# Performance work log

Measured on AMD Instinct MI355X. Metric: run time of the kernel, lower is better.

## Reference

```python
import jax, jax.numpy as jnp
import numpy as np

N_NODES = 100000
N_EDGES = 1600000
IN_CH = 256
OUT_CH = 128
EPS = 1e-12


def setup_inputs() -> dict:
    key = jax.random.key(0)
    k1, k2, k3 = jax.random.split(key, 3)
    x = jax.random.normal(k1, (N_NODES, IN_CH), dtype=jnp.float32)
    edge_index = jax.random.randint(k2, (2, N_EDGES), 0, N_NODES, dtype=jnp.int64)
    W = jax.random.normal(k3, (IN_CH, OUT_CH), dtype=jnp.float32) / np.float32(np.sqrt(IN_CH))
    b = jnp.zeros((OUT_CH,), dtype=jnp.float32)
    return {"x": x, "edge_index": edge_index, "W": W, "b": b}


def reference(x, edge_index, W, b):
    n = x.shape[0]
    # GCNConv: linear transform first, then normalized aggregation with self-loops
    h = x @ W  # [N, out]
    loops = jnp.arange(n, dtype=edge_index.dtype)
    row = jnp.concatenate([edge_index[0], loops])  # source nodes
    col = jnp.concatenate([edge_index[1], loops])  # destination nodes
    deg = jax.ops.segment_sum(jnp.ones_like(col, dtype=h.dtype), col, num_segments=n)
    dinv = jnp.where(deg > 0, jax.lax.rsqrt(jnp.maximum(deg, 1.0)), 0.0)  # deg^-1/2, inf->0
    wgt = dinv[row] * dinv[col]  # symmetric normalization per edge
    agg = jax.ops.segment_sum(h[row] * wgt[:, None], col, num_segments=n) + b  # [N, out]
    # min-max scale per node (dim=1)
    zmin = agg.min(axis=1, keepdims=True)
    zmax = agg.max(axis=1, keepdims=True)
    z = (agg - zmin) / (zmax - zmin)
    # F.normalize: L2 along dim=1 with eps clamp
    nrm = jnp.maximum(jnp.linalg.norm(z, axis=1, keepdims=True), EPS)
    return z / nrm
```

## Files before the change

kernel.cpp:

```cpp
#include <hip/hip_runtime.h>
#include <hip/hip_bf16.h>

#define N_NODES 100000
#define N_EDGES 1600000
#define IN_CH 256
#define OUT_CH 128

#define BSZ 512
#define NBUCK 196
#define BCAP 9216
#define CSC 8192

#define GEMM_ROWS 32

typedef __attribute__((ext_vector_type(8))) short short8;
typedef __attribute__((ext_vector_type(4))) float floatx4;
typedef __attribute__((ext_vector_type(2))) float float2v;

union bfu { __hip_bfloat16 b; unsigned short u; };

__device__ inline unsigned short f2bf(float v) {
    bfu cv; cv.b = __float2bfloat16(v); return cv.u;
}
__device__ inline float bf2f(unsigned short u) {
    bfu cv; cv.u = u; return __bfloat162float(cv.b);
}

__device__ inline void pkacc(float2v& acc, unsigned g) {
    float2v v;
    v.x = __uint_as_float(g << 16);
    v.y = __uint_as_float(g & 0xffff0000u);
    asm("v_pk_add_f32 %0, %1, %2" : "=v"(acc) : "v"(v), "v"(acc));
}

__global__ __launch_bounds__(256) void pa_scatter(const int* __restrict__ rows,
                                                  const int* __restrict__ cols,
                                                  int* __restrict__ bcursor,
                                                  unsigned* __restrict__ ebuf) {
    __shared__ int lcnt[NBUCK];
    __shared__ int lbase[NBUCK];
    int t = threadIdx.x;
    if (t < NBUCK) lcnt[t] = 0;
    __syncthreads();
    int s0 = blockIdx.x * CSC;
    int e1 = min(N_EDGES, s0 + CSC);
    for (int i = s0 + t; i < e1; i += 256) atomicAdd(&lcnt[cols[i] >> 9], 1);
    __syncthreads();
    if (t < NBUCK) {
        int c = lcnt[t];
        lbase[t] = c ? atomicAdd(&bcursor[t], c) : 0;
        lcnt[t] = 0;
    }
    __syncthreads();
    for (int i = s0 + t; i < e1; i += 256) {
        int c = cols[i], r = rows[i];
        int bk = c >> 9;
        int rank = atomicAdd(&lcnt[bk], 1);
        ebuf[bk * BCAP + lbase[bk] + rank] = ((unsigned)(c & (BSZ - 1)) << 17) | (unsigned)r;
    }
}

__global__ __launch_bounds__(256) void pb_build(const unsigned* __restrict__ ebuf,
                                                const int* __restrict__ bcursor,
                                                int* __restrict__ cnt,
                                                int* __restrict__ base,
                                                float* __restrict__ dinv,
                                                int* __restrict__ es) {
    __shared__ int nh[BSZ];
    __shared__ int sc[BSZ];
    __shared__ int lcur[BSZ];
    int t = threadIdx.x;
    int bk = blockIdx.x;
    int bb = bk * BCAP;
    int bc = bcursor[bk];
    nh[t] = 0; nh[t + 256] = 0;
    lcur[t] = 0; lcur[t + 256] = 0;
    __syncthreads();
    for (int i = t; i < bc; i += 256) atomicAdd(&nh[ebuf[bb + i] >> 17], 1);
    __syncthreads();
    sc[t] = nh[t]; sc[t + 256] = nh[t + 256];
    __syncthreads();
    for (int off = 1; off < BSZ; off <<= 1) {
        int v0 = (t >= off) ? sc[t - off] : 0;
        int i1 = t + 256;
        int v1 = (i1 >= off) ? sc[i1 - off] : 0;
        __syncthreads();
        sc[t] += v0; sc[i1] += v1;
        __syncthreads();
    }
#pragma unroll
    for (int q = 0; q < 2; ++q) {
        int dl = t + q * 256;
        int node = bk * BSZ + dl;
        if (node < N_NODES) {
            int c = nh[dl];
            cnt[node] = c;
            base[node] = bb + sc[dl] - c;
            dinv[node] = rsqrtf((float)(c + 1));
        }
    }
    for (int i = t; i < bc; i += 256) {
        unsigned v = ebuf[bb + i];
        int dl = v >> 17;
        int src = (int)(v & 0x1FFFFu);
        int rank = atomicAdd(&lcur[dl], 1);
        es[bb + sc[dl] - nh[dl] + rank] = src << 8;
    }
}

__global__ void k_prep_w(const float* __restrict__ W,
                         unsigned short* __restrict__ wb_hi,
                         unsigned short* __restrict__ wb_lo) {
    int t = blockIdx.x * 256 + threadIdx.x;
    if (t >= IN_CH * OUT_CH) return;
    int j = t & 7;
    int lane = (t >> 3) & 63;
    int s = (t >> 9) & 7;
    int nt = t >> 12;
    int k = s * 32 + (lane >> 4) * 8 + j;
    int n = nt * 16 + (lane & 15);
    float w = W[k * OUT_CH + n];
    unsigned short hi = f2bf(w);
    wb_hi[t] = hi;
    wb_lo[t] = f2bf(w - bf2f(hi));
}

__global__ __launch_bounds__(512) void k_gemm(const float* __restrict__ x,
                                              const unsigned short* __restrict__ wb_hi,
                                              const unsigned short* __restrict__ wb_lo,
                                              const float* __restrict__ dinv,
                                              unsigned short* __restrict__ hbs) {
    __shared__ short8 xbh[1024];
    __shared__ short8 xbl[1024];
    int t = threadIdx.x;
    int wv = t >> 6;
    int lane = t & 63;
    int row0 = blockIdx.x * GEMM_ROWS;

    short8 Bh[8], Bl[8];
    const short8* bhp = (const short8*)wb_hi + (size_t)wv * 8 * 64 + lane;
    const short8* blp = (const short8*)wb_lo + (size_t)wv * 8 * 64 + lane;
#pragma unroll
    for (int s = 0; s < 8; ++s) {
        Bh[s] = bhp[s * 64];
        Bl[s] = blp[s * 64];
    }

#pragma unroll
    for (int q = 0; q < 2; ++q) {
        int slot = q * 512 + t;
        int ms = slot >> 9;
        int s  = (slot >> 6) & 7;
        int l  = slot & 63;
        int row = row0 + ms * 16 + (l & 15);
        int col = s * 32 + (l >> 4) * 8;
        const float4* xp = (const float4*)(x + (size_t)row * IN_CH + col);
        float4 v0 = xp[0];
        float4 v1 = xp[1];
        float xv[8] = {v0.x, v0.y, v0.z, v0.w, v1.x, v1.y, v1.z, v1.w};
        short8 hh, ll;
#pragma unroll
        for (int j = 0; j < 8; ++j) {
            unsigned short hi = f2bf(xv[j]);
            hh[j] = (short)hi;
            ll[j] = (short)f2bf(xv[j] - bf2f(hi));
        }
        xbh[slot] = hh;
        xbl[slot] = ll;
    }
    __syncthreads();

    int r15 = lane & 15;
    int quad = lane >> 4;

    floatx4 acc[2];
#pragma unroll
    for (int ms = 0; ms < 2; ++ms) {
        acc[ms] = (floatx4){0.f, 0.f, 0.f, 0.f};
#pragma unroll
        for (int s = 0; s < 8; ++s) {
            short8 ah = xbh[(ms * 8 + s) * 64 + lane];
            short8 al = xbl[(ms * 8 + s) * 64 + lane];
            acc[ms] = __builtin_amdgcn_mfma_f32_16x16x32_bf16(ah, Bh[s], acc[ms], 0, 0, 0);
            acc[ms] = __builtin_amdgcn_mfma_f32_16x16x32_bf16(ah, Bl[s], acc[ms], 0, 0, 0);
            acc[ms] = __builtin_amdgcn_mfma_f32_16x16x32_bf16(al, Bh[s], acc[ms], 0, 0, 0);
        }
    }

#pragma unroll
    for (int ms = 0; ms < 2; ++ms)
#pragma unroll
        for (int r = 0; r < 4; ++r) {
            int row = row0 + ms * 16 + quad * 4 + r;
            size_t idx = (size_t)row * OUT_CH + wv * 16 + r15;
            hbs[idx] = f2bf(acc[ms][r] * dinv[row]);
        }
}

__global__ __launch_bounds__(256) void k_agg_fin(const unsigned short* __restrict__ hbs,
                                                 const float* __restrict__ dinv,
                                                 const int* __restrict__ es,
                                                 const int* __restrict__ base,
                                                 const int* __restrict__ cnt,
                                                 const float* __restrict__ b,
                                                 float* __restrict__ out) {
    int t = threadIdx.x;
    int lane = t & 63;
    int ll = lane & 15;
    int node = blockIdx.x * 16 + (t >> 4);

    const char* hb = (const char*)hbs;
    int lane_byte = ll << 4;
    int bidx = (lane & 48) << 2;

    float dn = dinv[node];
    int d  = cnt[node];
    int st = base[node];

    float4 bv0 = ((const float4*)b)[ll * 2];
    float4 bv1 = ((const float4*)b)[ll * 2 + 1];

    uint4 gs = *(const uint4*)(hb + ((size_t)node << 8) + lane_byte);
    float2v acc[4];
    acc[0].x = __uint_as_float(gs.x << 16); acc[0].y = __uint_as_float(gs.x & 0xffff0000u);
    acc[1].x = __uint_as_float(gs.y << 16); acc[1].y = __uint_as_float(gs.y & 0xffff0000u);
    acc[2].x = __uint_as_float(gs.z << 16); acc[2].y = __uint_as_float(gs.z & 0xffff0000u);
    acc[3].x = __uint_as_float(gs.w << 16); acc[3].y = __uint_as_float(gs.w & 0xffff0000u);

    int dm = d;
    dm = max(dm, __shfl_xor(dm, 16, 64));
    dm = max(dm, __shfl_xor(dm, 32, 64));
    int iters = __builtin_amdgcn_readfirstlane((dm + 15) >> 4);

    const int zoff = N_NODES << 8;

    for (int it = 0; it < iters; ++it) {
        int jb = it << 4;
        int off = zoff;
        if (jb + ll < d) off = es[st + jb + ll];

        uint4 ga[4], gb[4];
#pragma unroll
        for (int k = 0; k < 4; ++k) {
            int ro = __builtin_amdgcn_ds_bpermute(bidx + (k << 2), off);
            ga[k] = *(const uint4*)(hb + (unsigned)(ro + lane_byte));
        }
#pragma unroll
        for (int k = 0; k < 4; ++k) {
            int ro = __builtin_amdgcn_ds_bpermute(bidx + ((4 + k) << 2), off);
            gb[k] = *(const uint4*)(hb + (unsigned)(ro + lane_byte));
        }
#pragma unroll
        for (int k = 0; k < 4; ++k) {
            pkacc(acc[0], ga[k].x); pkacc(acc[1], ga[k].y);
            pkacc(acc[2], ga[k].z); pkacc(acc[3], ga[k].w);
        }
#pragma unroll
        for (int k = 0; k < 4; ++k) {
            int ro = __builtin_amdgcn_ds_bpermute(bidx + ((8 + k) << 2), off);
            ga[k] = *(const uint4*)(hb + (unsigned)(ro + lane_byte));
        }
#pragma unroll
        for (int k = 0; k < 4; ++k) {
            pkacc(acc[0], gb[k].x); pkacc(acc[1], gb[k].y);
            pkacc(acc[2], gb[k].z); pkacc(acc[3], gb[k].w);
        }
#pragma unroll
        for (int k = 0; k < 4; ++k) {
            int ro = __builtin_amdgcn_ds_bpermute(bidx + ((12 + k) << 2), off);
            gb[k] = *(const uint4*)(hb + (unsigned)(ro + lane_byte));
        }
#pragma unroll
        for (int k = 0; k < 4; ++k) {
            pkacc(acc[0], ga[k].x); pkacc(acc[1], ga[k].y);
            pkacc(acc[2], ga[k].z); pkacc(acc[3], ga[k].w);
        }
#pragma unroll
        for (int k = 0; k < 4; ++k) {
            pkacc(acc[0], gb[k].x); pkacc(acc[1], gb[k].y);
            pkacc(acc[2], gb[k].z); pkacc(acc[3], gb[k].w);
        }
    }

    float v[8];
    v[0] = dn * acc[0].x + bv0.x;  v[1] = dn * acc[0].y + bv0.y;
    v[2] = dn * acc[1].x + bv0.z;  v[3] = dn * acc[1].y + bv0.w;
    v[4] = dn * acc[2].x + bv1.x;  v[5] = dn * acc[2].y + bv1.y;
    v[6] = dn * acc[3].x + bv1.z;  v[7] = dn * acc[3].y + bv1.w;

    float lmin = v[0], lmax = v[0];
#pragma unroll
    for (int i = 1; i < 8; ++i) { lmin = fminf(lmin, v[i]); lmax = fmaxf(lmax, v[i]); }
#pragma unroll
    for (int m = 8; m; m >>= 1) {
        lmin = fminf(lmin, __shfl_xor(lmin, m, 64));
        lmax = fmaxf(lmax, __shfl_xor(lmax, m, 64));
    }
    float scale = 1.0f / (lmax - lmin);
    float z[8];
    float ss = 0.f;
#pragma unroll
    for (int i = 0; i < 8; ++i) { z[i] = (v[i] - lmin) * scale; ss += z[i] * z[i]; }
#pragma unroll
    for (int m = 8; m; m >>= 1) ss += __shfl_xor(ss, m, 64);
    float inv = 1.0f / fmaxf(sqrtf(ss), 1e-12f);

    float4 o0 = {z[0] * inv, z[1] * inv, z[2] * inv, z[3] * inv};
    float4 o1 = {z[4] * inv, z[5] * inv, z[6] * inv, z[7] * inv};
    float4* op = (float4*)(out + (size_t)node * OUT_CH);
    op[ll * 2] = o0;
    op[ll * 2 + 1] = o1;
}

extern "C" void kernel_launch(void* const* d_in, const int* in_sizes, int n_in,
                              void* d_out, int out_size, void* d_ws, size_t ws_size,
                              hipStream_t stream) {
    const float* x = (const float*)d_in[0];
    const int* ei = (const int*)d_in[1];
    const float* W = (const float*)d_in[2];
    const float* b = (const float*)d_in[3];
    float* out = (float*)d_out;

    char* ws = (char*)d_ws;
    size_t o = 0;
    auto alloc = [&](size_t bytes) { void* p = ws + o; o = (o + bytes + 255) & ~(size_t)255; return p; };
    float* dinv    = (float*)alloc((size_t)N_NODES * 4);
    int*   cnt     = (int*)  alloc((size_t)N_NODES * 4);
    int*   base    = (int*)  alloc((size_t)N_NODES * 4);
    int*   bcursor = (int*)  alloc(NBUCK * 4);
    unsigned short* wb_hi = (unsigned short*)alloc((size_t)IN_CH * OUT_CH * 2);
    unsigned short* wb_lo = (unsigned short*)alloc((size_t)IN_CH * OUT_CH * 2);
    unsigned short* hbs = (unsigned short*)alloc((size_t)(N_NODES + 1) * OUT_CH * 2);
    unsigned* ebuf = (unsigned*)alloc((size_t)NBUCK * BCAP * 4);
    int*   es      = (int*)  alloc((size_t)NBUCK * BCAP * 4);

    const int* rows = ei;
    const int* cols = ei + N_EDGES;

    hipMemsetAsync(bcursor, 0, NBUCK * sizeof(int), stream);
    hipMemsetAsync(hbs + (size_t)N_NODES * OUT_CH, 0, OUT_CH * 2, stream);
    pa_scatter<<<(N_EDGES + CSC - 1) / CSC, 256, 0, stream>>>(rows, cols, bcursor, ebuf);
    pb_build<<<NBUCK, 256, 0, stream>>>(ebuf, bcursor, cnt, base, dinv, es);

    k_prep_w<<<(IN_CH * OUT_CH + 255) / 256, 256, 0, stream>>>(W, wb_hi, wb_lo);
    k_gemm<<<N_NODES / GEMM_ROWS, 512, 0, stream>>>(x, wb_hi, wb_lo, dinv, hbs);

    k_agg_fin<<<N_NODES / 16, 256, 0, stream>>>(hbs, dinv, es, base, cnt, b, out);
}
```

Baseline: 307.4 us.

## Shrink CSR buckets, fold memsets into prep kernel, pad GEMM LDS tile

Halves the bucket size used to build the destination-sorted edge list (391 buckets of 256 nodes) and runs the scatter and build kernels with 512 threads, which gives more parallel blocks in the build stage. The two hipMemsetAsync calls are replaced by zeroing bcursor and the padding row inside k_prep_w, which now runs first and removes extra stream operations. The GEMM now loads x rows with coalesced contiguous reads and stores them into a padded LDS layout (stride 17 per quad) to avoid bank conflicts on the MFMA operand reads. In exchange, smaller buckets mean more global atomics on the bucket cursors, and the GEMM uses slightly more shared memory.

Result: faster. 284.2 us (-7.6%).

```diff
diff --git a/kernel.cpp b/kernel.cpp
--- a/kernel.cpp
+++ b/kernel.cpp
@@ -6,10 +6,10 @@
 #define IN_CH 256
 #define OUT_CH 128
 
-#define BSZ 512
-#define NBUCK 196
-#define BCAP 9216
-#define CSC 8192
+#define BSZ 256
+#define NBUCK 391
+#define BCAP 4736
+#define CSC 4096
 
 #define GEMM_ROWS 32
 
@@ -33,7 +33,33 @@
     asm("v_pk_add_f32 %0, %1, %2" : "=v"(acc) : "v"(v), "v"(acc));
 }
 
-__global__ __launch_bounds__(256) void pa_scatter(const int* __restrict__ rows,
+__global__ void k_prep_w(const float* __restrict__ W,
+                         unsigned short* __restrict__ wb_hi,
+                         unsigned short* __restrict__ wb_lo,
+                         int* __restrict__ bcursor,
+                         unsigned* __restrict__ zrow) {
+    int tid = threadIdx.x;
+    if (blockIdx.x == 0) {
+        if (tid < NBUCK) bcursor[tid] = 0;
+        if (tid + 256 < NBUCK) bcursor[tid + 256] = 0;
+    }
+    if (blockIdx.x == 1 && tid < 64) zrow[tid] = 0;
+
+    int t = blockIdx.x * 256 + tid;
+    if (t >= IN_CH * OUT_CH) return;
+    int j = t & 7;
+    int lane = (t >> 3) & 63;
+    int s = (t >> 9) & 7;
+    int nt = t >> 12;
+    int k = s * 32 + (lane >> 4) * 8 + j;
+    int n = nt * 16 + (lane & 15);
+    float w = W[k * OUT_CH + n];
+    unsigned short hi = f2bf(w);
+    wb_hi[t] = hi;
+    wb_lo[t] = f2bf(w - bf2f(hi));
+}
+
+__global__ __launch_bounds__(512) void pa_scatter(const int* __restrict__ rows,
                                                   const int* __restrict__ cols,
                                                   int* __restrict__ bcursor,
                                                   unsigned* __restrict__ ebuf) {
@@ -44,7 +70,7 @@
     __syncthreads();
     int s0 = blockIdx.x * CSC;
     int e1 = min(N_EDGES, s0 + CSC);
-    for (int i = s0 + t; i < e1; i += 256) atomicAdd(&lcnt[cols[i] >> 9], 1);
+    for (int i = s0 + t; i < e1; i += 512) atomicAdd(&lcnt[cols[i] >> 8], 1);
     __syncthreads();
     if (t < NBUCK) {
         int c = lcnt[t];
@@ -52,15 +78,15 @@
         lcnt[t] = 0;
     }
     __syncthreads();
-    for (int i = s0 + t; i < e1; i += 256) {
+    for (int i = s0 + t; i < e1; i += 512) {
         int c = cols[i], r = rows[i];
-        int bk = c >> 9;
+        int bk = c >> 8;
         int rank = atomicAdd(&lcnt[bk], 1);
         ebuf[bk * BCAP + lbase[bk] + rank] = ((unsigned)(c & (BSZ - 1)) << 17) | (unsigned)r;
     }
 }
 
-__global__ __launch_bounds__(256) void pb_build(const unsigned* __restrict__ ebuf,
+__global__ __launch_bounds__(512) void pb_build(const unsigned* __restrict__ ebuf,
                                                 const int* __restrict__ bcursor,
                                                 int* __restrict__ cnt,
                                                 int* __restrict__ base,
@@ -73,33 +99,28 @@
     int bk = blockIdx.x;
     int bb = bk * BCAP;
     int bc = bcursor[bk];
-    nh[t] = 0; nh[t + 256] = 0;
-    lcur[t] = 0; lcur[t + 256] = 0;
-    __syncthreads();
-    for (int i = t; i < bc; i += 256) atomicAdd(&nh[ebuf[bb + i] >> 17], 1);
-    __syncthreads();
-    sc[t] = nh[t]; sc[t + 256] = nh[t + 256];
+    if (t < BSZ) { nh[t] = 0; lcur[t] = 0; }
+    __syncthreads();
+    for (int i = t; i < bc; i += 512) atomicAdd(&nh[ebuf[bb + i] >> 17], 1);
+    __syncthreads();
+    if (t < BSZ) sc[t] = nh[t];
     __syncthreads();
     for (int off = 1; off < BSZ; off <<= 1) {
-        int v0 = (t >= off) ? sc[t - off] : 0;
-        int i1 = t + 256;
-        int v1 = (i1 >= off) ? sc[i1 - off] : 0;
+        int v = (t < BSZ && t >= off) ? sc[t - off] : 0;
         __syncthreads();
-        sc[t] += v0; sc[i1] += v1;
+        if (t < BSZ) sc[t] += v;
         __syncthreads();
     }
-#pragma unroll
-    for (int q = 0; q < 2; ++q) {
-        int dl = t + q * 256;
-        int node = bk * BSZ + dl;
+    if (t < BSZ) {
+        int node = bk * BSZ + t;
         if (node < N_NODES) {
-            int c = nh[dl];
+            int c = nh[t];
             cnt[node] = c;
-            base[node] = bb + sc[dl] - c;
+            base[node] = bb + sc[t] - c;
             dinv[node] = rsqrtf((float)(c + 1));
         }
     }
-    for (int i = t; i < bc; i += 256) {
+    for (int i = t; i < bc; i += 512) {
         unsigned v = ebuf[bb + i];
         int dl = v >> 17;
         int src = (int)(v & 0x1FFFFu);
@@ -108,30 +129,13 @@
     }
 }
 
-__global__ void k_prep_w(const float* __restrict__ W,
-                         unsigned short* __restrict__ wb_hi,
-                         unsigned short* __restrict__ wb_lo) {
-    int t = blockIdx.x * 256 + threadIdx.x;
-    if (t >= IN_CH * OUT_CH) return;
-    int j = t & 7;
-    int lane = (t >> 3) & 63;
-    int s = (t >> 9) & 7;
-    int nt = t >> 12;
-    int k = s * 32 + (lane >> 4) * 8 + j;
-    int n = nt * 16 + (lane & 15);
-    float w = W[k * OUT_CH + n];
-    unsigned short hi = f2bf(w);
-    wb_hi[t] = hi;
-    wb_lo[t] = f2bf(w - bf2f(hi));
-}
-
 __global__ __launch_bounds__(512) void k_gemm(const float* __restrict__ x,
                                               const unsigned short* __restrict__ wb_hi,
                                               const unsigned short* __restrict__ wb_lo,
                                               const float* __restrict__ dinv,
                                               unsigned short* __restrict__ hbs) {
-    __shared__ short8 xbh[1024];
-    __shared__ short8 xbl[1024];
+    __shared__ short8 xbh[2 * 8 * 68];
+    __shared__ short8 xbl[2 * 8 * 68];
     int t = threadIdx.x;
     int wv = t >> 6;
     int lane = t & 63;
@@ -148,13 +152,10 @@
 
 #pragma unroll
     for (int q = 0; q < 2; ++q) {
-        int slot = q * 512 + t;
-        int ms = slot >> 9;
-        int s  = (slot >> 6) & 7;
-        int l  = slot & 63;
-        int row = row0 + ms * 16 + (l & 15);
-        int col = s * 32 + (l >> 4) * 8;
-        const float4* xp = (const float4*)(x + (size_t)row * IN_CH + col);
+        int c = q * 512 + t;
+        int row = c >> 5;
+        int cc  = c & 31;
+        const float4* xp = (const float4*)(x + (size_t)(row0 + row) * IN_CH + cc * 8);
         float4 v0 = xp[0];
         float4 v1 = xp[1];
         float xv[8] = {v0.x, v0.y, v0.z, v0.w, v1.x, v1.y, v1.z, v1.w};
@@ -165,13 +166,16 @@
             hh[j] = (short)hi;
             ll[j] = (short)f2bf(xv[j] - bf2f(hi));
         }
-        xbh[slot] = hh;
-        xbl[slot] = ll;
+        int ms = row >> 4, r15 = row & 15, s = cc >> 2, q2 = cc & 3;
+        int idx = (ms * 8 + s) * 68 + q2 * 17 + r15;
+        xbh[idx] = hh;
+        xbl[idx] = ll;
     }
     __syncthreads();
 
     int r15 = lane & 15;
     int quad = lane >> 4;
+    int lidx = quad * 17 + r15;
 
     floatx4 acc[2];
 #pragma unroll
@@ -179,8 +183,8 @@
         acc[ms] = (floatx4){0.f, 0.f, 0.f, 0.f};
 #pragma unroll
         for (int s = 0; s < 8; ++s) {
-            short8 ah = xbh[(ms * 8 + s) * 64 + lane];
-            short8 al = xbl[(ms * 8 + s) * 64 + lane];
+            short8 ah = xbh[(ms * 8 + s) * 68 + lidx];
+            short8 al = xbl[(ms * 8 + s) * 68 + lidx];
             acc[ms] = __builtin_amdgcn_mfma_f32_16x16x32_bf16(ah, Bh[s], acc[ms], 0, 0, 0);
             acc[ms] = __builtin_amdgcn_mfma_f32_16x16x32_bf16(ah, Bl[s], acc[ms], 0, 0, 0);
             acc[ms] = __builtin_amdgcn_mfma_f32_16x16x32_bf16(al, Bh[s], acc[ms], 0, 0, 0);
@@ -337,12 +341,12 @@
     const int* rows = ei;
     const int* cols = ei + N_EDGES;
 
-    hipMemsetAsync(bcursor, 0, NBUCK * sizeof(int), stream);
-    hipMemsetAsync(hbs + (size_t)N_NODES * OUT_CH, 0, OUT_CH * 2, stream);
-    pa_scatter<<<(N_EDGES + CSC - 1) / CSC, 256, 0, stream>>>(rows, cols, bcursor, ebuf);
-    pb_build<<<NBUCK, 256, 0, stream>>>(ebuf, bcursor, cnt, base, dinv, es);
-
-    k_prep_w<<<(IN_CH * OUT_CH + 255) / 256, 256, 0, stream>>>(W, wb_hi, wb_lo);
+    k_prep_w<<<(IN_CH * OUT_CH + 255) / 256, 256, 0, stream>>>(
+        W, wb_hi, wb_lo, bcursor, (unsigned*)(hbs + (size_t)N_NODES * OUT_CH));
+
+    pa_scatter<<<(N_EDGES + CSC - 1) / CSC, 512, 0, stream>>>(rows, cols, bcursor, ebuf);
+    pb_build<<<NBUCK, 512, 0, stream>>>(ebuf, bcursor, cnt, base, dinv, es);
+
     k_gemm<<<N_NODES / GEMM_ROWS, 512, 0, stream>>>(x, wb_hi, wb_lo, dinv, hbs);
 
     k_agg_fin<<<N_NODES / 16, 256, 0, stream>>>(hbs, dinv, es, base, cnt, b, out);
```
